# Kernel tuning notes

Measured on AMD Instinct MI355X. Metric: run time of the kernel, lower is better.

Reference implementation:

```python
import jax, jax.numpy as jnp
import numpy as np

B, C, Q, E = 32, 1024, 64, 256  # batch, max_context_len, max_question_len, embedding_size
FE = 4 * E                      # final_encoding_size (self_attention=False)


def setup_inputs() -> dict:
    key = jax.random.key(0)
    ks = jax.random.split(key, 7)
    return {
        "context": jax.random.normal(ks[0], (B, C, E), dtype=jnp.float32),
        "question": jax.random.normal(ks[1], (B, Q, E), dtype=jnp.float32),
        "context_mask": jnp.ones((B, C), dtype=jnp.float32),
        "w_question": jax.random.normal(ks[2], (E,), dtype=jnp.float32),
        "w_context": jax.random.normal(ks[3], (E,), dtype=jnp.float32),
        "w_multiple": jax.random.normal(ks[4], (E,), dtype=jnp.float32),
        "final_W": jax.random.normal(ks[5], (FE, FE), dtype=jnp.float32) * (1.0 / np.sqrt(FE)),
        "final_b": jnp.zeros((FE,), dtype=jnp.float32),
    }


def reference(context, question, context_mask, w_question, w_context, w_multiple, final_W, final_b):
    # Trilinear similarity: s[b,c,q] = <w_q, q_q> + <w_c, c_c> + <w_m, c_c * q_q>
    q_weighted = question @ w_question                 # (B, Q)
    ctx_weighted = context @ w_context                 # (B, C)
    # (question.unsqueeze(1) * context.unsqueeze(2)) @ w_multiple, computed
    # without materializing the (B, C, Q, E) intermediate:
    mult = jnp.einsum('bce,bqe->bcq', context * w_multiple, question)  # (B, C, Q)
    similarity = ctx_weighted[:, :, None] + q_weighted[:, None, :] + mult  # (B, C, Q)

    # Context-to-query attention (softmax over question dim)
    c2q_att = jnp.einsum('bcq,bqe->bce', jax.nn.softmax(similarity, axis=2), question)

    # Query-to-context attention (softmax over context dim of row-max scores)
    q2c_weights = jax.nn.softmax(jnp.max(similarity, axis=2), axis=1)   # (B, C)
    q2c_att = jnp.einsum('bc,bce->be', q2c_weights, context)            # (B, E)

    attended = jnp.concatenate(
        [context, c2q_att, context * c2q_att, context * q2c_att[:, None, :]],
        axis=2)                                                          # (B, C, 4E)

    # MaskedLinear: affine map, output rows zeroed where context_mask == 0
    out = (attended @ final_W.T + final_b) * context_mask[:, :, None]    # (B, C, 4E)
    return out
```

## Files before the change

kernel.cpp:

```cpp
#include <hip/hip_runtime.h>

#define BB 32
#define CC 1024
#define QQ 64
#define EE 256
#define FE 1024
#define MM (BB*CC)

typedef __bf16 bf16_t;
typedef bf16_t bf16x8 __attribute__((ext_vector_type(8)));
typedef float f32x4 __attribute__((ext_vector_type(4)));
typedef unsigned short u16x8 __attribute__((ext_vector_type(8)));

__device__ __forceinline__ unsigned short f2bf(float f) {
  unsigned u = __float_as_uint(f);
  u += 0x7fffu + ((u >> 16) & 1u);
  return (unsigned short)(u >> 16);
}
__device__ __forceinline__ float bf2f(unsigned short u) {
  return __uint_as_float(((unsigned)u) << 16);
}

__device__ __forceinline__ void gload_lds16(const void* g, void* l) {
  __builtin_amdgcn_global_load_lds(
      (const __attribute__((address_space(1))) unsigned int*)g,
      (__attribute__((address_space(3))) unsigned int*)l, 16, 0, 0);
}

__global__ void k_prep(const float* __restrict__ question, const float* __restrict__ w_question,
                       float* __restrict__ qw,
                       const float* __restrict__ W, unsigned short* __restrict__ Wb) {
  int bx = blockIdx.x;
  if (bx < 512) {
    int gid = bx * 256 + threadIdx.x;
    int row = gid >> 6;
    int lane = gid & 63;
    const float4 q = *(const float4*)(question + (size_t)row * EE + lane * 4);
    const float4 wq = *(const float4*)(w_question + lane * 4);
    float d = q.x*wq.x + q.y*wq.y + q.z*wq.z + q.w*wq.w;
    d += __shfl_xor(d, 1);  d += __shfl_xor(d, 2);  d += __shfl_xor(d, 4);
    d += __shfl_xor(d, 8);  d += __shfl_xor(d, 16); d += __shfl_xor(d, 32);
    if (lane == 0) qw[row] = d;
  } else {
    int i = ((bx - 512) * 256 + threadIdx.x) * 4;
    float4 v = *(const float4*)(W + i);
    ushort4 o; o.x = f2bf(v.x); o.y = f2bf(v.y); o.z = f2bf(v.z); o.w = f2bf(v.w);
    *(ushort4*)(Wb + i) = o;
  }
}

#define DOT4(acc, A, Bv) acc += A.x*Bv.x + A.y*Bv.y + A.z*Bv.z + A.w*Bv.w

__launch_bounds__(256)
__global__ void k_simpv(const float* __restrict__ ctx, const float* __restrict__ question,
                        const float* __restrict__ qw_g, const float* __restrict__ w_context,
                        const float* __restrict__ w_multiple,
                        float* __restrict__ rowmax, unsigned short* __restrict__ att) {
  __shared__ float qbuf[QQ * 132];
  __shared__ float ck[64][36];
  __shared__ unsigned short Pl[QQ][68];
  __shared__ float cwl[64];
  __shared__ float qwl[QQ];
  const int tid = threadIdx.x;
  const int b = blockIdx.y;
  const int c0 = blockIdx.x * 64;
  const int tx = tid & 15, ty = tid >> 4;

  const float* qb = question + (size_t)b * (QQ * EE);
  if (tid < QQ) qwl[tid] = qw_g[b * QQ + tid];

  const int cr = tid >> 3, er = (tid & 7) * 4;
  const float* crow0 = ctx + ((size_t)(b * CC + c0 + cr)) * EE;
  const float* crow1 = crow0 + 32 * EE;
  unsigned short* arow0 = att + ((size_t)(b * CC + c0 + cr)) * FE;
  unsigned short* arow1 = arow0 + (size_t)32 * FE;
  float s[4][4] = {{0.f}};
  float cp0 = 0.f, cp1 = 0.f;

  for (int h = 0; h < 2; ++h) {
    if (h) __syncthreads();
    for (int idx = tid * 4; idx < QQ * 128; idx += 1024) {
      int row = idx >> 7, col = idx & 127;
      *(float4*)&qbuf[row * 132 + col] = *(const float4*)(qb + (size_t)row * EE + h * 128 + col);
    }
    for (int eo2 = 0; eo2 < 128; eo2 += 32) {
      const int eo = h * 128 + eo2;
      float4 cv0 = *(const float4*)(crow0 + eo + er);
      float4 cv1 = *(const float4*)(crow1 + eo + er);
      float4 wc = *(const float4*)(w_context + eo + er);
      float4 wm = *(const float4*)(w_multiple + eo + er);
      cp0 += cv0.x*wc.x + cv0.y*wc.y + cv0.z*wc.z + cv0.w*wc.w;
      cp1 += cv1.x*wc.x + cv1.y*wc.y + cv1.z*wc.z + cv1.w*wc.w;
      ushort4 u0, u1;
      u0.x = f2bf(cv0.x); u0.y = f2bf(cv0.y); u0.z = f2bf(cv0.z); u0.w = f2bf(cv0.w);
      u1.x = f2bf(cv1.x); u1.y = f2bf(cv1.y); u1.z = f2bf(cv1.z); u1.w = f2bf(cv1.w);
      *(ushort4*)(arow0 + eo + er) = u0;
      *(ushort4*)(arow1 + eo + er) = u1;
      __syncthreads();
      float4 m0, m1;
      m0.x = cv0.x*wm.x; m0.y = cv0.y*wm.y; m0.z = cv0.z*wm.z; m0.w = cv0.w*wm.w;
      m1.x = cv1.x*wm.x; m1.y = cv1.y*wm.y; m1.z = cv1.z*wm.z; m1.w = cv1.w*wm.w;
      *(float4*)&ck[cr][er] = m0;
      *(float4*)&ck[cr + 32][er] = m1;
      __syncthreads();
#pragma unroll
      for (int ee = 0; ee < 32; ee += 4) {
        float4 a0 = *(const float4*)&ck[ty +  0][ee];
        float4 a1 = *(const float4*)&ck[ty + 16][ee];
        float4 a2 = *(const float4*)&ck[ty + 32][ee];
        float4 a3 = *(const float4*)&ck[ty + 48][ee];
        float4 b0 = *(const float4*)&qbuf[(tx +  0) * 132 + eo2 + ee];
        float4 b1 = *(const float4*)&qbuf[(tx + 16) * 132 + eo2 + ee];
        float4 b2 = *(const float4*)&qbuf[(tx + 32) * 132 + eo2 + ee];
        float4 b3 = *(const float4*)&qbuf[(tx + 48) * 132 + eo2 + ee];
        DOT4(s[0][0], a0, b0); DOT4(s[0][1], a0, b1); DOT4(s[0][2], a0, b2); DOT4(s[0][3], a0, b3);
        DOT4(s[1][0], a1, b0); DOT4(s[1][1], a1, b1); DOT4(s[1][2], a1, b2); DOT4(s[1][3], a1, b3);
        DOT4(s[2][0], a2, b0); DOT4(s[2][1], a2, b1); DOT4(s[2][2], a2, b2); DOT4(s[2][3], a2, b3);
        DOT4(s[3][0], a3, b0); DOT4(s[3][1], a3, b1); DOT4(s[3][2], a3, b2); DOT4(s[3][3], a3, b3);
      }
    }
  }
  cp0 += __shfl_xor(cp0, 1); cp0 += __shfl_xor(cp0, 2); cp0 += __shfl_xor(cp0, 4);
  cp1 += __shfl_xor(cp1, 1); cp1 += __shfl_xor(cp1, 2); cp1 += __shfl_xor(cp1, 4);
  if ((tid & 7) == 0) { cwl[cr] = cp0; cwl[cr + 32] = cp1; }
  __syncthreads();

#pragma unroll
  for (int i = 0; i < 4; ++i) {
    int c = ty + 16 * i;
    float cw = cwl[c];
    float f[4], mx = -1e30f;
#pragma unroll
    for (int j = 0; j < 4; ++j) {
      f[j] = s[i][j] + cw + qwl[tx + 16 * j];
      mx = fmaxf(mx, f[j]);
    }
    mx = fmaxf(mx, __shfl_xor(mx, 1));
    mx = fmaxf(mx, __shfl_xor(mx, 2));
    mx = fmaxf(mx, __shfl_xor(mx, 4));
    mx = fmaxf(mx, __shfl_xor(mx, 8));
    float sum = 0.f;
#pragma unroll
    for (int j = 0; j < 4; ++j) { f[j] = expf(f[j] - mx); sum += f[j]; }
    sum += __shfl_xor(sum, 1);
    sum += __shfl_xor(sum, 2);
    sum += __shfl_xor(sum, 4);
    sum += __shfl_xor(sum, 8);
    float inv = 1.f / sum;
    if (tx == 0) rowmax[(size_t)b * CC + c0 + c] = mx;
#pragma unroll
    for (int j = 0; j < 4; ++j) Pl[tx + 16 * j][c] = f2bf(f[j] * inv);
  }
  __syncthreads();

  for (int ep = 0; ep < EE; ep += 64) {
    if (ep) __syncthreads();
    {
      int q = tid >> 2, e16 = (tid & 3) * 16;
      const float* src = qb + (size_t)q * EE + ep + e16;
      *(float4*)&qbuf[q * 68 + e16 +  0] = *(const float4*)(src);
      *(float4*)&qbuf[q * 68 + e16 +  4] = *(const float4*)(src + 4);
      *(float4*)&qbuf[q * 68 + e16 +  8] = *(const float4*)(src + 8);
      *(float4*)&qbuf[q * 68 + e16 + 12] = *(const float4*)(src + 12);
    }
    __syncthreads();
    float s2[4][4] = {{0.f}};
#pragma unroll 8
    for (int q = 0; q < QQ; ++q) {
      float a0 = bf2f(Pl[q][ty +  0]);
      float a1 = bf2f(Pl[q][ty + 16]);
      float a2 = bf2f(Pl[q][ty + 32]);
      float a3 = bf2f(Pl[q][ty + 48]);
      float4 bv = *(const float4*)&qbuf[q * 68 + tx * 4];
      s2[0][0] += a0 * bv.x; s2[0][1] += a0 * bv.y; s2[0][2] += a0 * bv.z; s2[0][3] += a0 * bv.w;
      s2[1][0] += a1 * bv.x; s2[1][1] += a1 * bv.y; s2[1][2] += a1 * bv.z; s2[1][3] += a1 * bv.w;
      s2[2][0] += a2 * bv.x; s2[2][1] += a2 * bv.y; s2[2][2] += a2 * bv.z; s2[2][3] += a2 * bv.w;
      s2[3][0] += a3 * bv.x; s2[3][1] += a3 * bv.y; s2[3][2] += a3 * bv.z; s2[3][3] += a3 * bv.w;
    }
#pragma unroll
    for (int i = 0; i < 4; ++i) {
      int c = ty + 16 * i;
      size_t row = (size_t)(b * CC + c0 + c);
      unsigned short* arow = att + row * (size_t)FE;
      ushort4 cu = *(const ushort4*)(arow + ep + tx * 4);
      float cx = bf2f(cu.x), cy = bf2f(cu.y), cz = bf2f(cu.z), cw = bf2f(cu.w);
      ushort4 o1, o2;
      o1.x = f2bf(s2[i][0]);       o1.y = f2bf(s2[i][1]);       o1.z = f2bf(s2[i][2]);       o1.w = f2bf(s2[i][3]);
      o2.x = f2bf(cx * s2[i][0]);  o2.y = f2bf(cy * s2[i][1]);  o2.z = f2bf(cz * s2[i][2]);  o2.w = f2bf(cw * s2[i][3]);
      *(ushort4*)(arow + 1 * EE + ep + tx * 4) = o1;
      *(ushort4*)(arow + 2 * EE + ep + tx * 4) = o2;
    }
  }
}

__global__ void k_q2c_softmax(const float* __restrict__ rowmax, float* __restrict__ q2cw) {
  int b = blockIdx.x, tid = threadIdx.x;
  __shared__ float rbuf[4], sbuf[4];
  float4 v = *(const float4*)(rowmax + (size_t)b * CC + tid * 4);
  float m = fmaxf(fmaxf(v.x, v.y), fmaxf(v.z, v.w));
  for (int off = 1; off < 64; off <<= 1) m = fmaxf(m, __shfl_xor(m, off));
  int wv = tid >> 6;
  if ((tid & 63) == 0) rbuf[wv] = m;
  __syncthreads();
  m = fmaxf(fmaxf(rbuf[0], rbuf[1]), fmaxf(rbuf[2], rbuf[3]));
  float e0 = expf(v.x - m), e1 = expf(v.y - m), e2 = expf(v.z - m), e3 = expf(v.w - m);
  float sum = e0 + e1 + e2 + e3;
  for (int off = 1; off < 64; off <<= 1) sum += __shfl_xor(sum, off);
  if ((tid & 63) == 0) sbuf[wv] = sum;
  __syncthreads();
  sum = sbuf[0] + sbuf[1] + sbuf[2] + sbuf[3];
  float inv = 1.f / sum;
  float4 o; o.x = e0 * inv; o.y = e1 * inv; o.z = e2 * inv; o.w = e3 * inv;
  *(float4*)(q2cw + (size_t)b * CC + tid * 4) = o;
}

__global__ void k_q2c_part(const unsigned short* __restrict__ att, const float* __restrict__ w,
                           float* __restrict__ part) {
  int b = blockIdx.y, ch = blockIdx.x;
  int e = threadIdx.x;
  const unsigned short* base = att + ((size_t)(b * CC + ch * 128)) * FE + e;
  const float* wp = w + b * CC + ch * 128;
  float acc = 0.f;
#pragma unroll 4
  for (int c = 0; c < 128; ++c) acc += wp[c] * bf2f(base[(size_t)c * FE]);
  part[(b * 8 + ch) * EE + e] = acc;
}

__launch_bounds__(256, 3)
__global__ void k_gemm(const unsigned short* __restrict__ A, const unsigned short* __restrict__ Bw,
                       const float* __restrict__ part, const float* __restrict__ bias,
                       const float* __restrict__ mask, float* __restrict__ out) {
  __shared__ bf16_t As[128][32];
  __shared__ bf16_t Bs[128][32];
  __shared__ float q2cl[EE];
  const int tid = threadIdx.x;
  const int lane = tid & 63;
  const int wave = tid >> 6;
  const int wr = wave >> 1, wc = wave & 1;

  const int bid = blockIdx.x;
  const int wg = (bid & 7) * 256 + (bid >> 3);
  const int bcol = (wg & 7) * 128;
  const int brow = (wg >> 3) * 128;
  const int bb = brow >> 10;

  const int r = lane & 15, kg = lane >> 4;
  const int rk = (kg ^ (r & 3)) * 8;

  const int srow = tid >> 2;
  const int sgr = tid & 3;
  const int ssw = (sgr ^ (srow & 3)) * 8;
  const unsigned short* gA0 = A  + (size_t)(brow + srow) * FE + ssw;
  const unsigned short* gA1 = gA0 + (size_t)64 * FE;
  const unsigned short* gB0 = Bw + (size_t)(bcol + srow) * FE + ssw;
  const unsigned short* gB1 = gB0 + (size_t)64 * FE;
  bf16_t* dA0 = &As[srow][sgr * 8];
  bf16_t* dA1 = dA0 + 64 * 32;
  bf16_t* dB0 = &Bs[srow][sgr * 8];
  bf16_t* dB1 = dB0 + 64 * 32;

  {
    float a = 0.f;
#pragma unroll
    for (int ch = 0; ch < 8; ++ch) a += part[(bb * 8 + ch) * EE + tid];
    q2cl[tid] = a;
  }

  f32x4 acc[4][4] = {};

  for (int k0 = 0; k0 < FE; k0 += 32) {
    if (k0 < 768) {
      gload_lds16(gA0 + k0, dA0);
      gload_lds16(gA1 + k0, dA1);
    } else {
      const int e0 = k0 - 768;
      u16x8 va = *(const u16x8*)(gA0 + e0);
      u16x8 vb = *(const u16x8*)(gA1 + e0);
      float4 g0 = *(const float4*)&q2cl[e0 + ssw];
      float4 g1 = *(const float4*)&q2cl[e0 + ssw + 4];
      u16x8 oa, ob;
      oa[0] = f2bf(bf2f(va[0]) * g0.x); oa[1] = f2bf(bf2f(va[1]) * g0.y);
      oa[2] = f2bf(bf2f(va[2]) * g0.z); oa[3] = f2bf(bf2f(va[3]) * g0.w);
      oa[4] = f2bf(bf2f(va[4]) * g1.x); oa[5] = f2bf(bf2f(va[5]) * g1.y);
      oa[6] = f2bf(bf2f(va[6]) * g1.z); oa[7] = f2bf(bf2f(va[7]) * g1.w);
      ob[0] = f2bf(bf2f(vb[0]) * g0.x); ob[1] = f2bf(bf2f(vb[1]) * g0.y);
      ob[2] = f2bf(bf2f(vb[2]) * g0.z); ob[3] = f2bf(bf2f(vb[3]) * g0.w);
      ob[4] = f2bf(bf2f(vb[4]) * g1.x); ob[5] = f2bf(bf2f(vb[5]) * g1.y);
      ob[6] = f2bf(bf2f(vb[6]) * g1.z); ob[7] = f2bf(bf2f(vb[7]) * g1.w);
      *(u16x8*)dA0 = oa;
      *(u16x8*)dA1 = ob;
    }
    gload_lds16(gB0 + k0, dB0);
    gload_lds16(gB1 + k0, dB1);
    __syncthreads();
    bf16x8 fa[4], fb[4];
#pragma unroll
    for (int m = 0; m < 4; ++m) fa[m] = *(const bf16x8*)&As[wr * 64 + m * 16 + r][rk];
#pragma unroll
    for (int n = 0; n < 4; ++n) fb[n] = *(const bf16x8*)&Bs[wc * 64 + n * 16 + r][rk];
#pragma unroll
    for (int m = 0; m < 4; ++m)
#pragma unroll
      for (int n = 0; n < 4; ++n)
        acc[m][n] = __builtin_amdgcn_mfma_f32_16x16x32_bf16(fa[m], fb[n], acc[m][n], 0, 0, 0);
    __syncthreads();
  }

#pragma unroll
  for (int m = 0; m < 4; ++m) {
#pragma unroll
    for (int n = 0; n < 4; ++n) {
#pragma unroll
      for (int reg = 0; reg < 4; ++reg) {
        int row = brow + wr * 64 + m * 16 + kg * 4 + reg;
        int col = bcol + wc * 64 + n * 16 + r;
        out[(size_t)row * FE + col] = (acc[m][n][reg] + bias[col]) * mask[row];
      }
    }
  }
}

extern "C" void kernel_launch(void* const* d_in, const int* in_sizes, int n_in,
                              void* d_out, int out_size, void* d_ws, size_t ws_size,
                              hipStream_t stream) {
  const float* ctx  = (const float*)d_in[0];
  const float* ques = (const float*)d_in[1];
  const float* mask = (const float*)d_in[2];
  const float* w_q  = (const float*)d_in[3];
  const float* w_c  = (const float*)d_in[4];
  const float* w_m  = (const float*)d_in[5];
  const float* fW   = (const float*)d_in[6];
  const float* fb   = (const float*)d_in[7];
  float* out = (float*)d_out;

  char* ws = (char*)d_ws;
  float* qw     = (float*)(ws);
  float* rowmax = (float*)(ws + 8192);
  float* q2cw   = (float*)(ws + 139264);
  float* part   = (float*)(ws + 270336);
  unsigned short* attended = (unsigned short*)(ws + 1048576);
  unsigned short* Wb       = (unsigned short*)(ws + 68157440);

  k_prep<<<1536, 256, 0, stream>>>(ques, w_q, qw, fW, Wb);
  k_simpv<<<dim3(16, 32), 256, 0, stream>>>(ctx, ques, qw, w_c, w_m, rowmax, attended);
  k_q2c_softmax<<<32, 256, 0, stream>>>(rowmax, q2cw);
  k_q2c_part<<<dim3(8, 32), 256, 0, stream>>>(attended, q2cw, part);
  k_gemm<<<2048, 256, 0, stream>>>(attended, Wb, part, fb, mask, out);
}
```

Baseline: 168.8 us.

## Enlarge GEMM tile to 256x128 with K step 64 and 8-way LDS swizzle

The final projection GEMM now computes a 256x128 output tile per block, with each wave holding 8x4 MFMA accumulators, and steps K by 64 instead of 32, with a wider XOR swizzle in LDS. The aim is more reuse of each loaded A/B fragment and half as many barriers per unit of K work. In exchange, the kernel uses more registers and LDS, drops to 2 blocks per CU and launches half as many blocks, which lowers occupancy and latency hiding.

```diff
diff --git a/kernel.cpp b/kernel.cpp
--- a/kernel.cpp
+++ b/kernel.cpp
@@ -226,12 +226,12 @@
   part[(b * 8 + ch) * EE + e] = acc;
 }
 
-__launch_bounds__(256, 3)
+__launch_bounds__(256, 2)
 __global__ void k_gemm(const unsigned short* __restrict__ A, const unsigned short* __restrict__ Bw,
                        const float* __restrict__ part, const float* __restrict__ bias,
                        const float* __restrict__ mask, float* __restrict__ out) {
-  __shared__ bf16_t As[128][32];
-  __shared__ bf16_t Bs[128][32];
+  __shared__ bf16_t As[256][64];
+  __shared__ bf16_t Bs[128][64];
   __shared__ float q2cl[EE];
   const int tid = threadIdx.x;
   const int lane = tid & 63;
@@ -239,25 +239,20 @@
   const int wr = wave >> 1, wc = wave & 1;
 
   const int bid = blockIdx.x;
-  const int wg = (bid & 7) * 256 + (bid >> 3);
+  const int wg = (bid & 7) * 128 + (bid >> 3);
   const int bcol = (wg & 7) * 128;
-  const int brow = (wg >> 3) * 128;
+  const int brow = (wg >> 3) * 256;
   const int bb = brow >> 10;
 
   const int r = lane & 15, kg = lane >> 4;
-  const int rk = (kg ^ (r & 3)) * 8;
-
-  const int srow = tid >> 2;
-  const int sgr = tid & 3;
-  const int ssw = (sgr ^ (srow & 3)) * 8;
-  const unsigned short* gA0 = A  + (size_t)(brow + srow) * FE + ssw;
-  const unsigned short* gA1 = gA0 + (size_t)64 * FE;
-  const unsigned short* gB0 = Bw + (size_t)(bcol + srow) * FE + ssw;
-  const unsigned short* gB1 = gB0 + (size_t)64 * FE;
-  bf16_t* dA0 = &As[srow][sgr * 8];
-  bf16_t* dA1 = dA0 + 64 * 32;
-  bf16_t* dB0 = &Bs[srow][sgr * 8];
-  bf16_t* dB1 = dB0 + 64 * 32;
+  const int rx = r & 7;
+
+  const int srow = tid >> 3;
+  const int ssw = ((tid & 7) ^ (srow & 7)) * 8;
+  const unsigned short* gA = A  + (size_t)(brow + srow) * FE + ssw;
+  const unsigned short* gB = Bw + (size_t)(bcol + srow) * FE + ssw;
+  bf16_t* dA = (bf16_t*)As + tid * 8;
+  bf16_t* dB = (bf16_t*)Bs + tid * 8;
 
   {
     float a = 0.f;
@@ -266,53 +261,58 @@
     q2cl[tid] = a;
   }
 
-  f32x4 acc[4][4] = {};
-
-  for (int k0 = 0; k0 < FE; k0 += 32) {
+  f32x4 acc[8][4] = {};
+
+  for (int k0 = 0; k0 < FE; k0 += 64) {
     if (k0 < 768) {
-      gload_lds16(gA0 + k0, dA0);
-      gload_lds16(gA1 + k0, dA1);
+#pragma unroll
+      for (int i = 0; i < 8; ++i)
+        gload_lds16(gA + (size_t)(i * 32) * FE + k0, dA + i * 2048);
     } else {
       const int e0 = k0 - 768;
-      u16x8 va = *(const u16x8*)(gA0 + e0);
-      u16x8 vb = *(const u16x8*)(gA1 + e0);
       float4 g0 = *(const float4*)&q2cl[e0 + ssw];
       float4 g1 = *(const float4*)&q2cl[e0 + ssw + 4];
-      u16x8 oa, ob;
-      oa[0] = f2bf(bf2f(va[0]) * g0.x); oa[1] = f2bf(bf2f(va[1]) * g0.y);
-      oa[2] = f2bf(bf2f(va[2]) * g0.z); oa[3] = f2bf(bf2f(va[3]) * g0.w);
-      oa[4] = f2bf(bf2f(va[4]) * g1.x); oa[5] = f2bf(bf2f(va[5]) * g1.y);
-      oa[6] = f2bf(bf2f(va[6]) * g1.z); oa[7] = f2bf(bf2f(va[7]) * g1.w);
-      ob[0] = f2bf(bf2f(vb[0]) * g0.x); ob[1] = f2bf(bf2f(vb[1]) * g0.y);
-      ob[2] = f2bf(bf2f(vb[2]) * g0.z); ob[3] = f2bf(bf2f(vb[3]) * g0.w);
-      ob[4] = f2bf(bf2f(vb[4]) * g1.x); ob[5] = f2bf(bf2f(vb[5]) * g1.y);
-      ob[6] = f2bf(bf2f(vb[6]) * g1.z); ob[7] = f2bf(bf2f(vb[7]) * g1.w);
-      *(u16x8*)dA0 = oa;
-      *(u16x8*)dA1 = ob;
-    }
-    gload_lds16(gB0 + k0, dB0);
-    gload_lds16(gB1 + k0, dB1);
+#pragma unroll
+      for (int i = 0; i < 8; ++i) {
+        u16x8 v = *(const u16x8*)(gA + (size_t)(i * 32) * FE + e0);
+        u16x8 o;
+        o[0] = f2bf(bf2f(v[0]) * g0.x); o[1] = f2bf(bf2f(v[1]) * g0.y);
+        o[2] = f2bf(bf2f(v[2]) * g0.z); o[3] = f2bf(bf2f(v[3]) * g0.w);
+        o[4] = f2bf(bf2f(v[4]) * g1.x); o[5] = f2bf(bf2f(v[5]) * g1.y);
+        o[6] = f2bf(bf2f(v[6]) * g1.z); o[7] = f2bf(bf2f(v[7]) * g1.w);
+        *(u16x8*)(dA + i * 2048) = o;
+      }
+    }
+#pragma unroll
+    for (int i = 0; i < 4; ++i)
+      gload_lds16(gB + (size_t)(i * 32) * FE + k0, dB + i * 2048);
     __syncthreads();
-    bf16x8 fa[4], fb[4];
-#pragma unroll
-    for (int m = 0; m < 4; ++m) fa[m] = *(const bf16x8*)&As[wr * 64 + m * 16 + r][rk];
-#pragma unroll
-    for (int n = 0; n < 4; ++n) fb[n] = *(const bf16x8*)&Bs[wc * 64 + n * 16 + r][rk];
-#pragma unroll
-    for (int m = 0; m < 4; ++m)
+
+#pragma unroll
+    for (int ks = 0; ks < 2; ++ks) {
+      bf16x8 fa[8], fb[4];
+#pragma unroll
+      for (int m = 0; m < 8; ++m)
+        fa[m] = *(const bf16x8*)&As[wr * 128 + m * 16 + r][((ks * 4 + kg) ^ rx) * 8];
 #pragma unroll
       for (int n = 0; n < 4; ++n)
-        acc[m][n] = __builtin_amdgcn_mfma_f32_16x16x32_bf16(fa[m], fb[n], acc[m][n], 0, 0, 0);
+        fb[n] = *(const bf16x8*)&Bs[wc * 64 + n * 16 + r][((ks * 4 + kg) ^ rx) * 8];
+#pragma unroll
+      for (int m = 0; m < 8; ++m)
+#pragma unroll
+        for (int n = 0; n < 4; ++n)
+          acc[m][n] = __builtin_amdgcn_mfma_f32_16x16x32_bf16(fa[m], fb[n], acc[m][n], 0, 0, 0);
+    }
     __syncthreads();
   }
 
 #pragma unroll
-  for (int m = 0; m < 4; ++m) {
+  for (int m = 0; m < 8; ++m) {
 #pragma unroll
     for (int n = 0; n < 4; ++n) {
 #pragma unroll
       for (int reg = 0; reg < 4; ++reg) {
-        int row = brow + wr * 64 + m * 16 + kg * 4 + reg;
+        int row = brow + wr * 128 + m * 16 + kg * 4 + reg;
         int col = bcol + wc * 64 + n * 16 + r;
         out[(size_t)row * FE + col] = (acc[m][n][reg] + bias[col]) * mask[row];
       }
@@ -345,5 +345,5 @@
   k_simpv<<<dim3(16, 32), 256, 0, stream>>>(ctx, ques, qw, w_c, w_m, rowmax, attended);
   k_q2c_softmax<<<32, 256, 0, stream>>>(rowmax, q2cw);
   k_q2c_part<<<dim3(8, 32), 256, 0, stream>>>(attended, q2cw, part);
-  k_gemm<<<2048, 256, 0, stream>>>(attended, Wb, part, fb, mask, out);
-}
+  k_gemm<<<1024, 256, 0, stream>>>(attended, Wb, part, fb, mask, out);
+}
```

Measured after the change: 157.8 us. 1.07x faster.
